# Kernel tuning notes

Measured on AMD Instinct MI355X. Metric: run time of the kernel, lower is better.

Reference implementation:

```python
import jax, jax.numpy as jnp
import numpy as np

N_NODES = 40000
N_EDGES = 640000
D_FEAT = 128
HIDDEN = 128
N_GRAPHS = 512


def setup_inputs() -> dict:
    key = jax.random.key(0)
    ks = jax.random.split(key, 6)
    x = jax.random.normal(ks[0], (N_NODES, D_FEAT), dtype=jnp.float32)
    edge_index = jax.random.randint(ks[1], (2, N_EDGES), 0, N_NODES, dtype=jnp.int32)
    batch = jnp.sort(jax.random.randint(ks[2], (N_NODES,), 0, N_GRAPHS, dtype=jnp.int32))
    s1 = 1.0 / np.sqrt(D_FEAT)
    s2 = 1.0 / np.sqrt(HIDDEN)
    W1 = jax.random.normal(ks[3], (D_FEAT, HIDDEN), dtype=jnp.float32) * s1
    b1 = jnp.zeros((HIDDEN,), dtype=jnp.float32)
    W2 = jax.random.normal(ks[4], (HIDDEN, HIDDEN), dtype=jnp.float32) * s2
    b2 = jnp.zeros((HIDDEN,), dtype=jnp.float32)
    Wfc = jax.random.normal(ks[5], (HIDDEN, 1), dtype=jnp.float32) * s2
    bfc = jnp.zeros((1,), dtype=jnp.float32)
    return {"x": x, "edge_index": edge_index, "batch": batch,
            "W1": W1, "b1": b1, "W2": W2, "b2": b2, "Wfc": Wfc, "bfc": bfc}


def _gcn_conv(x, edge_index, W, b):
    # PyG GCNConv: linear transform, add self-loops, symmetric deg^{-1/2} norm,
    # scatter-add messages from row (source) to col (target), then bias.
    n = x.shape[0]
    h = x @ W  # [N, H]
    row, col = edge_index[0], edge_index[1]
    ones = jnp.ones_like(col, dtype=h.dtype)
    deg = 1.0 + jax.ops.segment_sum(ones, col, num_segments=n)  # self-loop included
    dinv = jax.lax.rsqrt(deg)  # [N]
    norm = dinv[row] * dinv[col]  # [E]
    msg = h[row] * norm[:, None]  # [E, H]
    out = jax.ops.segment_sum(msg, col, num_segments=n)
    out = out + h * (dinv * dinv)[:, None]  # self-loop contribution
    return out + b


def _mean_pool(x, batch, num_graphs):
    sums = jax.ops.segment_sum(x, batch, num_segments=num_graphs)
    cnt = jax.ops.segment_sum(jnp.ones((x.shape[0],), dtype=x.dtype), batch, num_segments=num_graphs)
    return sums / jnp.maximum(cnt, 1.0)[:, None]


def reference(x, edge_index, batch, W1, b1, W2, b2, Wfc, bfc):
    h = jax.nn.relu(_gcn_conv(x, edge_index, W1, b1))
    h = jax.nn.relu(_gcn_conv(h, edge_index, W2, b2))
    g = _mean_pool(h, batch, N_GRAPHS)  # [G, H]
    return g @ Wfc + bfc  # [G, 1]
```

## Files before the change

### kernel.cpp

```cpp
#include <hip/hip_runtime.h>
#include <hip/hip_fp16.h>

#define N_NODES 40000
#define N_EDGES 640000
#define NFEAT   128
#define N_GRAPHS 512
#define SCAN_NB 157
#define NBKT    157
#define BKT_CAP 8192
#define BIN_BLK_EDGES 2048
#define NBLK_A ((N_EDGES + BIN_BLK_EDGES - 1) / BIN_BLK_EDGES)
#define EPAD_MAX (N_EDGES + 7 * N_NODES)

__global__ void init_misc_kernel(int* __restrict__ gcursor, int* __restrict__ gcnt,
                                 float* __restrict__ out, const float* __restrict__ bfc,
                                 __half* __restrict__ hsent) {
    int t = threadIdx.x;
    if (t <= NBKT) gcursor[t] = 0;
    float b = bfc[0];
    for (int i = t; i < N_GRAPHS; i += 256) { gcnt[i] = 0; out[i] = b; }
    if (t < NFEAT) hsent[t] = __float2half(0.0f);
}

__global__ __launch_bounds__(256) void bin_kernel(const int* __restrict__ ei,
                                                  int* __restrict__ gcursor,
                                                  unsigned int* __restrict__ binned) {
    __shared__ int lhist[NBKT];
    __shared__ int lbase[NBKT];
    const int t  = threadIdx.x;
    const int e0 = blockIdx.x * BIN_BLK_EDGES;

    if (t < NBKT) lhist[t] = 0;
    __syncthreads();

    int creg[BIN_BLK_EDGES / 256];
    #pragma unroll
    for (int i = 0; i < BIN_BLK_EDGES / 256; ++i) {
        int e = e0 + i * 256 + t;
        creg[i] = (e < N_EDGES) ? ei[N_EDGES + e] : -1;
        if (creg[i] >= 0) atomicAdd(&lhist[creg[i] >> 8], 1);
    }
    __syncthreads();

    if (t < NBKT) { lbase[t] = atomicAdd(&gcursor[t], lhist[t]); lhist[t] = 0; }
    __syncthreads();

    #pragma unroll
    for (int i = 0; i < BIN_BLK_EDGES / 256; ++i) {
        int c = creg[i];
        if (c >= 0) {
            int e = e0 + i * 256 + t;
            int r = ei[e];
            int bkt = c >> 8;
            int slot = atomicAdd(&lhist[bkt], 1);
            binned[(size_t)bkt * BKT_CAP + lbase[bkt] + slot] =
                (unsigned int)r | ((unsigned int)(c & 255) << 16);
        }
    }
}

template <typename IdxT>
__global__ __launch_bounds__(256) void bucket_build_kernel(const unsigned int* __restrict__ binned,
                                                           const int* __restrict__ gcursor,
                                                           int* __restrict__ gbase,
                                                           const int* __restrict__ batch,
                                                           int* __restrict__ gcnt,
                                                           float* __restrict__ dinv,
                                                           int* __restrict__ rowptr,
                                                           IdxT* __restrict__ csr) {
    __shared__ int chist[256];
    __shared__ int scn[256];
    __shared__ int ccur[256];
    __shared__ int ghist[N_GRAPHS];
    __shared__ int sbase;
    const int b = blockIdx.x, t = threadIdx.x;
    chist[t] = 0;
    ghist[t] = 0;
    ghist[t + 256] = 0;
    __syncthreads();
    const int cnt = gcursor[b];
    const unsigned int* src = binned + (size_t)b * BKT_CAP;
    const int col = b * 256 + t;
    const int valid = (col < N_NODES);
    if (valid) atomicAdd(&ghist[batch[col]], 1);
    for (int i = t; i < cnt; i += 256) atomicAdd(&chist[src[i] >> 16], 1);
    __syncthreads();
    int d = chist[t];
    if (valid) dinv[col] = rsqrtf(1.0f + (float)d);
    int pd = valid ? ((d + 7) & ~7) : 0;
    scn[t] = pd;
    __syncthreads();
    for (int off = 1; off < 256; off <<= 1) {
        int add = (t >= off) ? scn[t - off] : 0;
        __syncthreads();
        scn[t] += add;
        __syncthreads();
    }
    if (t == 255) sbase = atomicAdd(gbase, scn[255]);
    __syncthreads();
    const int start = sbase + scn[t] - pd;
    if (valid) rowptr[col] = start | ((pd >> 2) << 20);
    ccur[t] = start;
    __syncthreads();
    for (int i = t; i < cnt; i += 256) {
        unsigned int u = src[i];
        int slot = atomicAdd(&ccur[u >> 16], 1);
        csr[slot] = (IdxT)(u & 0xFFFFu);
    }
    __syncthreads();
    if (valid) {
        int cur = ccur[t];
        int endp = start + pd;
        for (int p = cur; p < endp; ++p) csr[p] = (IdxT)N_NODES;
    }
    int h0 = ghist[t], h1 = ghist[t + 256];
    if (h0) atomicAdd(&gcnt[t], h0);
    if (h1) atomicAdd(&gcnt[t + 256], h1);
}

__device__ inline float4 load_h4(const __half* p) {
    uint2 raw = *(const uint2*)p;
    __half2 h0 = *(__half2*)&raw.x;
    __half2 h1 = *(__half2*)&raw.y;
    float2 f0 = __half22float2(h0);
    float2 f1 = __half22float2(h1);
    return make_float4(f0.x, f0.y, f1.x, f1.y);
}
__device__ inline float4 load4v(const float* p)  { return *(const float4*)(p); }
__device__ inline float4 load4v(const __half* p) { return load_h4(p); }

__device__ inline void acc8(const uint4& raw, float* a) {
    float2 f;
    f = __half22float2(*(const __half2*)&raw.x); a[0] += f.x; a[1] += f.y;
    f = __half22float2(*(const __half2*)&raw.y); a[2] += f.x; a[3] += f.y;
    f = __half22float2(*(const __half2*)&raw.z); a[4] += f.x; a[5] += f.y;
    f = __half22float2(*(const __half2*)&raw.w); a[6] += f.x; a[7] += f.y;
}

__device__ inline int pick_q(ushort4 v, int q) {
    unsigned long long ul;
    __builtin_memcpy(&ul, &v, 8);
    return (int)((unsigned int)(ul >> (q << 4)) & 0xFFFFu);
}

template <typename InT>
__global__ __launch_bounds__(256, 4) void gemm64h_kernel(const InT* __restrict__ X,
                                                         const float* __restrict__ W,
                                                         const float* __restrict__ dinv,
                                                         __half* __restrict__ H) {
    __shared__ float Ws[128 * 64];
    const int colhalf = blockIdx.x & 1;
    const int tile    = blockIdx.x >> 1;

    for (int i = threadIdx.x; i < 2048; i += 256) {
        int k   = i >> 4;
        int cc4 = (i & 15) * 4;
        *(float4*)(Ws + k * 64 + cc4) = *(const float4*)(W + k * 128 + colhalf * 64 + cc4);
    }
    __syncthreads();

    const int rg = threadIdx.x >> 4;
    const int cg = threadIdx.x & 15;
    const int row0 = tile * 64 + rg * 4;
    const InT* x0 = X + (size_t)row0 * NFEAT;

    float acc[4][4] = {};
    float4 xc[4], xn[4];
    #pragma unroll
    for (int i = 0; i < 4; i++) xc[i] = load4v(x0 + (size_t)i * NFEAT);

    #pragma unroll 4
    for (int k = 0; k < 128; k += 4) {
        const int kn = (k + 4) & 127;
        #pragma unroll
        for (int i = 0; i < 4; i++) xn[i] = load4v(x0 + (size_t)i * NFEAT + kn);

        float4 wv[4];
        #pragma unroll
        for (int m = 0; m < 4; m++) wv[m] = *(const float4*)(Ws + (k + m) * 64 + cg * 4);

        #pragma unroll
        for (int i = 0; i < 4; i++) {
            const float xi[4] = {xc[i].x, xc[i].y, xc[i].z, xc[i].w};
            #pragma unroll
            for (int m = 0; m < 4; m++) {
                acc[i][0] += xi[m] * wv[m].x;
                acc[i][1] += xi[m] * wv[m].y;
                acc[i][2] += xi[m] * wv[m].z;
                acc[i][3] += xi[m] * wv[m].w;
            }
        }
        #pragma unroll
        for (int i = 0; i < 4; i++) xc[i] = xn[i];
    }

    #pragma unroll
    for (int i = 0; i < 4; i++) {
        float dr = dinv[row0 + i];
        __half2 p0 = __floats2half2_rn(acc[i][0] * dr, acc[i][1] * dr);
        __half2 p1 = __floats2half2_rn(acc[i][2] * dr, acc[i][3] * dr);
        uint2 pk;
        pk.x = *(unsigned int*)&p0;
        pk.y = *(unsigned int*)&p1;
        *(uint2*)(H + (size_t)(row0 + i) * NFEAT + colhalf * 64 + cg * 4) = pk;
    }
}

template <typename IdxT, typename IdxV, bool FUSE_POOL>
__global__ __launch_bounds__(256) void gather_w16_kernel(
        const int* __restrict__ rowptr, const IdxT* __restrict__ csr,
        const float* __restrict__ dinv, const __half* __restrict__ Ht,
        const float* __restrict__ bias, __half* __restrict__ outh,
        const float* __restrict__ Wfc, const int* __restrict__ batch,
        const int* __restrict__ gcnt, float* __restrict__ out, int n) {
    int gid  = blockIdx.x * blockDim.x + threadIdx.x;
    int node = __builtin_amdgcn_readfirstlane(gid >> 6);
    if (node >= n) return;
    int lane = threadIdx.x & 63;
    int q    = lane >> 4;
    int fo   = lane & 15;

    unsigned int u = (unsigned int)__builtin_amdgcn_readfirstlane(rowptr[node]);
    int start = (int)(u & 0xFFFFFu);
    int pd    = (int)(u >> 20) << 2;
    int end   = start + pd;

    float a[8] = {0.f, 0.f, 0.f, 0.f, 0.f, 0.f, 0.f, 0.f};

    if (q == 0) {
        uint4 raw = *(const uint4*)(Ht + (size_t)node * NFEAT + fo * 8);
        acc8(raw, a);
    }

    if (start < end) {
        IdxV n0 = *(const IdxV*)(csr + start);
        IdxV n1 = *(const IdxV*)(csr + start + 4);
        for (int j = start; j < end; j += 8) {
            IdxV c0 = n0, c1 = n1;
            int jn = j + 8;
            if (jn < end) {
                n0 = *(const IdxV*)(csr + jn);
                n1 = *(const IdxV*)(csr + jn + 4);
            }
            int ra = pick_q(c0, q);
            int rb = pick_q(c1, q);
            uint4 raw0 = *(const uint4*)(Ht + (size_t)ra * NFEAT + fo * 8);
            uint4 raw1 = *(const uint4*)(Ht + (size_t)rb * NFEAT + fo * 8);
            acc8(raw0, a);
            acc8(raw1, a);
        }
    }

    #pragma unroll
    for (int i = 0; i < 8; i++) {
        a[i] += __shfl_xor(a[i], 16, 64);
        a[i] += __shfl_xor(a[i], 32, 64);
    }

    float di = dinv[node];
    const float4 bb0 = *(const float4*)(bias + fo * 8);
    const float4 bb1 = *(const float4*)(bias + fo * 8 + 4);
    float o0 = fmaxf(a[0] * di + bb0.x, 0.0f);
    float o1 = fmaxf(a[1] * di + bb0.y, 0.0f);
    float o2 = fmaxf(a[2] * di + bb0.z, 0.0f);
    float o3 = fmaxf(a[3] * di + bb0.w, 0.0f);
    float o4 = fmaxf(a[4] * di + bb1.x, 0.0f);
    float o5 = fmaxf(a[5] * di + bb1.y, 0.0f);
    float o6 = fmaxf(a[6] * di + bb1.z, 0.0f);
    float o7 = fmaxf(a[7] * di + bb1.w, 0.0f);

    if (!FUSE_POOL) {
        if (q == 0) {
            __half2 p0 = __floats2half2_rn(o0, o1);
            __half2 p1 = __floats2half2_rn(o2, o3);
            __half2 p2 = __floats2half2_rn(o4, o5);
            __half2 p3 = __floats2half2_rn(o6, o7);
            uint4 pk;
            pk.x = *(unsigned int*)&p0;
            pk.y = *(unsigned int*)&p1;
            pk.z = *(unsigned int*)&p2;
            pk.w = *(unsigned int*)&p3;
            *(uint4*)(outh + (size_t)node * NFEAT + fo * 8) = pk;
        }
    } else {
        const float4 wf0 = *(const float4*)(Wfc + fo * 8);
        const float4 wf1 = *(const float4*)(Wfc + fo * 8 + 4);
        float dsum = o0 * wf0.x + o1 * wf0.y + o2 * wf0.z + o3 * wf0.w
                   + o4 * wf1.x + o5 * wf1.y + o6 * wf1.z + o7 * wf1.w;
        dsum += __shfl_xor(dsum, 1, 64);
        dsum += __shfl_xor(dsum, 2, 64);
        dsum += __shfl_xor(dsum, 4, 64);
        dsum += __shfl_xor(dsum, 8, 64);
        if (lane == 0) {
            int g = batch[node];
            int c = gcnt[g];
            float cf = (float)(c > 0 ? c : 1);
            atomicAdd(&out[g], dsum / cf);
        }
    }
}

__global__ void edge_deg_int_kernel(const int* __restrict__ ei, int* __restrict__ degcnt, int E) {
    int e = blockIdx.x * blockDim.x + threadIdx.x;
    if (e < E) atomicAdd(&degcnt[ei[E + e]], 1);
}

__global__ void dinv_from_int_kernel(const int* __restrict__ degcnt, float* __restrict__ dinv, int n) {
    int i = blockIdx.x * blockDim.x + threadIdx.x;
    if (i < n) dinv[i] = rsqrtf(1.0f + (float)degcnt[i]);
}

__global__ __launch_bounds__(256, 4) void gemm64f_kernel(const float* __restrict__ X,
                                                         const float* __restrict__ W,
                                                         const float* __restrict__ dinv,
                                                         float* __restrict__ H) {
    __shared__ float Ws[128 * 64];
    const int colhalf = blockIdx.x & 1;
    const int tile    = blockIdx.x >> 1;
    for (int i = threadIdx.x; i < 2048; i += 256) {
        int k   = i >> 4;
        int cc4 = (i & 15) * 4;
        *(float4*)(Ws + k * 64 + cc4) = *(const float4*)(W + k * 128 + colhalf * 64 + cc4);
    }
    __syncthreads();
    const int rg = threadIdx.x >> 4;
    const int cg = threadIdx.x & 15;
    const int row0 = tile * 64 + rg * 4;
    const float* x0 = X + (size_t)row0 * NFEAT;
    float acc[4][4] = {};
    #pragma unroll 4
    for (int k = 0; k < 128; k += 4) {
        float4 xv[4];
        float4 wv[4];
        #pragma unroll
        for (int i = 0; i < 4; i++) xv[i] = *(const float4*)(x0 + (size_t)i * NFEAT + k);
        #pragma unroll
        for (int m = 0; m < 4; m++) wv[m] = *(const float4*)(Ws + (k + m) * 64 + cg * 4);
        #pragma unroll
        for (int i = 0; i < 4; i++) {
            const float xi[4] = {xv[i].x, xv[i].y, xv[i].z, xv[i].w};
            #pragma unroll
            for (int m = 0; m < 4; m++) {
                acc[i][0] += xi[m] * wv[m].x;
                acc[i][1] += xi[m] * wv[m].y;
                acc[i][2] += xi[m] * wv[m].z;
                acc[i][3] += xi[m] * wv[m].w;
            }
        }
    }
    #pragma unroll
    for (int i = 0; i < 4; i++) {
        float dr = dinv[row0 + i];
        float4 o = {acc[i][0] * dr, acc[i][1] * dr, acc[i][2] * dr, acc[i][3] * dr};
        *(float4*)(H + (size_t)(row0 + i) * NFEAT + cg * 4 + colhalf * 64) = o;
    }
}

__global__ __launch_bounds__(256) void edge_scatter_kernel(const int* __restrict__ ei,
                                                           const float* __restrict__ dinv,
                                                           const float* __restrict__ H,
                                                           float* __restrict__ agg,
                                                           int E) {
    long long gid = (long long)blockIdx.x * blockDim.x + threadIdx.x;
    int e = (int)(gid >> 5);
    if (e >= E) return;
    int c4 = ((int)gid & 31) * 4;
    int r = ei[e];
    int c = ei[E + e];
    float norm = dinv[c];
    const float4 hv = *(const float4*)(H + (size_t)r * NFEAT + c4);
    float* dst = agg + (size_t)c * NFEAT + c4;
    atomicAdd(dst + 0, hv.x * norm);
    atomicAdd(dst + 1, hv.y * norm);
    atomicAdd(dst + 2, hv.z * norm);
    atomicAdd(dst + 3, hv.w * norm);
}

__global__ void post_kernel(float* __restrict__ agg, const float* __restrict__ H,
                            const float* __restrict__ dinv, const float* __restrict__ b,
                            int n) {
    int gid = blockIdx.x * blockDim.x + threadIdx.x;
    if (gid >= n * 32) return;
    int node = gid >> 5;
    int c4 = (gid & 31) * 4;
    float s = dinv[node];
    float4 a  = *(float4*)(agg + (size_t)gid * 4);
    float4 hv = *(const float4*)(H + (size_t)gid * 4);
    float4 bb = *(const float4*)(b + c4);
    float4 o;
    o.x = fmaxf(a.x + hv.x * s + bb.x, 0.0f);
    o.y = fmaxf(a.y + hv.y * s + bb.y, 0.0f);
    o.z = fmaxf(a.z + hv.z * s + bb.z, 0.0f);
    o.w = fmaxf(a.w + hv.w * s + bb.w, 0.0f);
    *(float4*)(agg + (size_t)gid * 4) = o;
}

__global__ __launch_bounds__(128) void pool_fc_kernel(const float* __restrict__ H,
                                                      const int* __restrict__ batch,
                                                      const float* __restrict__ Wfc,
                                                      const float* __restrict__ bfc,
                                                      float* __restrict__ out, int n) {
    int g = blockIdx.x;
    int tid = threadIdx.x;
    int lo = 0, hi = n;
    while (lo < hi) { int mid = (lo + hi) >> 1; if (batch[mid] < g) lo = mid + 1; else hi = mid; }
    int start = lo;
    hi = n;
    while (lo < hi) { int mid = (lo + hi) >> 1; if (batch[mid] < g + 1) lo = mid + 1; else hi = mid; }
    int end = lo;
    float acc = 0.0f;
    for (int nd = start; nd < end; ++nd) acc += H[(size_t)nd * NFEAT + tid];
    float cnt = (float)((end - start) > 0 ? (end - start) : 1);
    float v = (acc / cnt) * Wfc[tid];
    __shared__ float red[128];
    red[tid] = v;
    __syncthreads();
    #pragma unroll
    for (int s = 64; s > 0; s >>= 1) {
        if (tid < s) red[tid] += red[tid + s];
        __syncthreads();
    }
    if (tid == 0) out[g] = red[0] + bfc[0];
}

static void run_csr_path(const float* x, const int* ei, const int* batch,
                         const float* W1, const float* b1, const float* W2,
                         const float* b2, const float* Wfc, const float* bfc,
                         float* out, void* d_ws, hipStream_t stream) {
    typedef unsigned short IdxT;
    typedef ushort4 IdxV;
    char* ws = (char*)d_ws;
    const size_t hbytes = (size_t)(N_NODES + 1) * NFEAT * sizeof(__half);
    const size_t obytes = (size_t)N_NODES * NFEAT * sizeof(__half);
    __half* hbuf  = (__half*)ws;
    __half* obuf  = (__half*)(ws + hbytes);
    IdxT*   csr   = (IdxT*)(ws + hbytes + obytes);
    char*   p     = ws + hbytes + obytes + ((size_t)EPAD_MAX * sizeof(IdxT) + 15) / 16 * 16;
    int*    rowptr = (int*)p;                p += ((size_t)(N_NODES + 1) * 4 + 15) / 16 * 16;
    float*  dinv   = (float*)p;              p += ((size_t)N_NODES * 4 + 15) / 16 * 16;
    int*    gcnt   = (int*)p;

    unsigned int* binned = (unsigned int*)obuf;
    int* gcursor = (int*)(binned + (size_t)NBKT * BKT_CAP);

    init_misc_kernel<<<1, 256, 0, stream>>>(gcursor, gcnt, out, bfc,
                                            hbuf + (size_t)N_NODES * NFEAT);
    bin_kernel<<<NBLK_A, 256, 0, stream>>>(ei, gcursor, binned);
    bucket_build_kernel<IdxT><<<NBKT, 256, 0, stream>>>(binned, gcursor, gcursor + NBKT,
                                                        batch, gcnt, dinv, rowptr, csr);

    gemm64h_kernel<float><<<(N_NODES / 64) * 2, 256, 0, stream>>>(x, W1, dinv, hbuf);
    gather_w16_kernel<IdxT, IdxV, false><<<(N_NODES * 64) / 256, 256, 0, stream>>>(
        rowptr, csr, dinv, hbuf, b1, obuf, nullptr, nullptr, nullptr, nullptr, N_NODES);

    gemm64h_kernel<__half><<<(N_NODES / 64) * 2, 256, 0, stream>>>(obuf, W2, dinv, hbuf);
    gather_w16_kernel<IdxT, IdxV, true><<<(N_NODES * 64) / 256, 256, 0, stream>>>(
        rowptr, csr, dinv, hbuf, b2, nullptr, Wfc, batch, gcnt, out, N_NODES);
}

extern "C" void kernel_launch(void* const* d_in, const int* in_sizes, int n_in,
                              void* d_out, int out_size, void* d_ws, size_t ws_size,
                              hipStream_t stream) {
    const float* x     = (const float*)d_in[0];
    const int*   ei    = (const int*)  d_in[1];
    const int*   batch = (const int*)  d_in[2];
    const float* W1    = (const float*)d_in[3];
    const float* b1    = (const float*)d_in[4];
    const float* W2    = (const float*)d_in[5];
    const float* b2    = (const float*)d_in[6];
    const float* Wfc   = (const float*)d_in[7];
    const float* bfc   = (const float*)d_in[8];
    float* out = (float*)d_out;

    const size_t hbytes = (size_t)(N_NODES + 1) * NFEAT * sizeof(__half);
    const size_t obytes = (size_t)N_NODES * NFEAT * sizeof(__half);
    const size_t tail   = ((size_t)(N_NODES + 1) * 4 + 15) / 16 * 16
                        + ((size_t)N_NODES * 4 + 15) / 16 * 16
                        + (size_t)N_GRAPHS * 4;
    const size_t need = hbytes + obytes + ((size_t)EPAD_MAX * 2 + 15) / 16 * 16 + tail;

    if (ws_size >= need) {
        run_csr_path(x, ei, batch, W1, b1, W2, b2, Wfc, bfc, out, d_ws, stream);
    } else {
        float* ws   = (float*)d_ws;
        int*   degc = (int*)ws;
        float* dinv = ws + N_NODES;
        float* hbuf = ws + 2 * N_NODES;
        float* agg  = hbuf + (size_t)N_NODES * NFEAT;
        const size_t fb2 = (size_t)N_NODES * NFEAT * sizeof(float);

        hipMemsetAsync(degc, 0, (size_t)N_NODES * sizeof(int), stream);
        edge_deg_int_kernel<<<N_EDGES / 256, 256, 0, stream>>>(ei, degc, N_EDGES);
        dinv_from_int_kernel<<<SCAN_NB, 256, 0, stream>>>(degc, dinv, N_NODES);

        hipMemsetAsync(agg, 0, fb2, stream);
        gemm64f_kernel<<<(N_NODES / 64) * 2, 256, 0, stream>>>(x, W1, dinv, hbuf);
        edge_scatter_kernel<<<(N_EDGES * 32) / 256, 256, 0, stream>>>(ei, dinv, hbuf, agg, N_EDGES);
        post_kernel<<<(N_NODES * 32) / 256, 256, 0, stream>>>(agg, hbuf, dinv, b1, N_NODES);

        gemm64f_kernel<<<(N_NODES / 64) * 2, 256, 0, stream>>>(agg, W2, dinv, hbuf);
        hipMemsetAsync(agg, 0, fb2, stream);
        edge_scatter_kernel<<<(N_EDGES * 32) / 256, 256, 0, stream>>>(ei, dinv, hbuf, agg, N_EDGES);
        post_kernel<<<(N_NODES * 32) / 256, 256, 0, stream>>>(agg, hbuf, dinv, b2, N_NODES);

        pool_fc_kernel<<<N_GRAPHS, 128, 0, stream>>>(agg, batch, Wfc, bfc, out, N_NODES);
    }
}
```

Measured before the change: 276.5 us.

## Split gather kernels into four feature slabs across grid y dimension

The per-node neighbour gather now runs over four 32-feature slabs, one per blockIdx.y, with each wave handling 8 neighbours at once (8 lanes per neighbour, 4 halfs each) instead of 4 neighbours with 8 halfs per lane. This quadruples the wave count and shortens the per-node loop, aiming to raise memory-level parallelism and reduce load imbalance on high-degree nodes. In exchange, the CSR index and rowptr reads are repeated four times, each gather load shrinks to 8 bytes, and the fused pool issues four times as many atomics to the output.

Result: slower. 406.2 us (+46.9%).

```diff
diff --git a/kernel.cpp b/kernel.cpp
--- a/kernel.cpp
+++ b/kernel.cpp
@@ -11,6 +11,7 @@
 #define BIN_BLK_EDGES 2048
 #define NBLK_A ((N_EDGES + BIN_BLK_EDGES - 1) / BIN_BLK_EDGES)
 #define EPAD_MAX (N_EDGES + 7 * N_NODES)
+#define NSLAB 4
 
 __global__ void init_misc_kernel(int* __restrict__ gcursor, int* __restrict__ gcnt,
                                  float* __restrict__ out, const float* __restrict__ bfc,
@@ -129,18 +130,17 @@
 __device__ inline float4 load4v(const float* p)  { return *(const float4*)(p); }
 __device__ inline float4 load4v(const __half* p) { return load_h4(p); }
 
-__device__ inline void acc8(const uint4& raw, float* a) {
-    float2 f;
-    f = __half22float2(*(const __half2*)&raw.x); a[0] += f.x; a[1] += f.y;
-    f = __half22float2(*(const __half2*)&raw.y); a[2] += f.x; a[3] += f.y;
-    f = __half22float2(*(const __half2*)&raw.z); a[4] += f.x; a[5] += f.y;
-    f = __half22float2(*(const __half2*)&raw.w); a[6] += f.x; a[7] += f.y;
-}
-
-__device__ inline int pick_q(ushort4 v, int q) {
-    unsigned long long ul;
-    __builtin_memcpy(&ul, &v, 8);
-    return (int)((unsigned int)(ul >> (q << 4)) & 0xFFFFu);
+__device__ inline void acc4(uint2 raw, float& a0, float& a1, float& a2, float& a3) {
+    float2 f0 = __half22float2(*(__half2*)&raw.x);
+    float2 f1 = __half22float2(*(__half2*)&raw.y);
+    a0 += f0.x; a1 += f0.y; a2 += f1.x; a3 += f1.y;
+}
+
+__device__ inline int pick8(const uint4& v, int use_hi, int shift) {
+    unsigned long long lo = ((unsigned long long)v.y << 32) | (unsigned long long)v.x;
+    unsigned long long hi = ((unsigned long long)v.w << 32) | (unsigned long long)v.z;
+    unsigned long long sel = use_hi ? hi : lo;
+    return (int)((unsigned int)(sel >> shift) & 0xFFFFu);
 }
 
 template <typename InT>
@@ -206,91 +206,78 @@
     }
 }
 
-template <typename IdxT, typename IdxV, bool FUSE_POOL>
-__global__ __launch_bounds__(256) void gather_w16_kernel(
+template <typename IdxT, bool FUSE_POOL>
+__global__ __launch_bounds__(256) void gather_slab_kernel(
         const int* __restrict__ rowptr, const IdxT* __restrict__ csr,
         const float* __restrict__ dinv, const __half* __restrict__ Ht,
         const float* __restrict__ bias, __half* __restrict__ outh,
         const float* __restrict__ Wfc, const int* __restrict__ batch,
         const int* __restrict__ gcnt, float* __restrict__ out, int n) {
+    const int slab = blockIdx.y;
     int gid  = blockIdx.x * blockDim.x + threadIdx.x;
-    int node = __builtin_amdgcn_readfirstlane(gid >> 6);
+    int node = gid >> 6;
     if (node >= n) return;
     int lane = threadIdx.x & 63;
-    int q    = lane >> 4;
-    int fo   = lane & 15;
-
-    unsigned int u = (unsigned int)__builtin_amdgcn_readfirstlane(rowptr[node]);
+    int oct  = lane >> 3;
+    int fi   = lane & 7;
+    const int use_hi = oct >> 2;
+    const int shift  = (oct & 3) << 4;
+    const int fbase  = slab * 32 + fi * 4;
+    const __half* __restrict__ Hs = Ht + fbase;
+
+    unsigned int u = (unsigned int)rowptr[node];
     int start = (int)(u & 0xFFFFFu);
     int pd    = (int)(u >> 20) << 2;
     int end   = start + pd;
 
-    float a[8] = {0.f, 0.f, 0.f, 0.f, 0.f, 0.f, 0.f, 0.f};
-
-    if (q == 0) {
-        uint4 raw = *(const uint4*)(Ht + (size_t)node * NFEAT + fo * 8);
-        acc8(raw, a);
+    float a0 = 0.f, a1 = 0.f, a2 = 0.f, a3 = 0.f;
+
+    if (oct == 0) {
+        uint2 raw = *(const uint2*)(Hs + (size_t)node * NFEAT);
+        acc4(raw, a0, a1, a2, a3);
     }
 
     if (start < end) {
-        IdxV n0 = *(const IdxV*)(csr + start);
-        IdxV n1 = *(const IdxV*)(csr + start + 4);
+        uint4 iv = *(const uint4*)(csr + start);
         for (int j = start; j < end; j += 8) {
-            IdxV c0 = n0, c1 = n1;
+            uint4 cv = iv;
             int jn = j + 8;
-            if (jn < end) {
-                n0 = *(const IdxV*)(csr + jn);
-                n1 = *(const IdxV*)(csr + jn + 4);
-            }
-            int ra = pick_q(c0, q);
-            int rb = pick_q(c1, q);
-            uint4 raw0 = *(const uint4*)(Ht + (size_t)ra * NFEAT + fo * 8);
-            uint4 raw1 = *(const uint4*)(Ht + (size_t)rb * NFEAT + fo * 8);
-            acc8(raw0, a);
-            acc8(raw1, a);
-        }
-    }
-
-    #pragma unroll
-    for (int i = 0; i < 8; i++) {
-        a[i] += __shfl_xor(a[i], 16, 64);
-        a[i] += __shfl_xor(a[i], 32, 64);
-    }
+            if (jn < end) iv = *(const uint4*)(csr + jn);
+            int r = pick8(cv, use_hi, shift);
+            uint2 raw = *(const uint2*)(Hs + (size_t)r * NFEAT);
+            acc4(raw, a0, a1, a2, a3);
+        }
+    }
+
+    a0 += __shfl_xor(a0, 8, 64);  a1 += __shfl_xor(a1, 8, 64);
+    a2 += __shfl_xor(a2, 8, 64);  a3 += __shfl_xor(a3, 8, 64);
+    a0 += __shfl_xor(a0, 16, 64); a1 += __shfl_xor(a1, 16, 64);
+    a2 += __shfl_xor(a2, 16, 64); a3 += __shfl_xor(a3, 16, 64);
+    a0 += __shfl_xor(a0, 32, 64); a1 += __shfl_xor(a1, 32, 64);
+    a2 += __shfl_xor(a2, 32, 64); a3 += __shfl_xor(a3, 32, 64);
 
     float di = dinv[node];
-    const float4 bb0 = *(const float4*)(bias + fo * 8);
-    const float4 bb1 = *(const float4*)(bias + fo * 8 + 4);
-    float o0 = fmaxf(a[0] * di + bb0.x, 0.0f);
-    float o1 = fmaxf(a[1] * di + bb0.y, 0.0f);
-    float o2 = fmaxf(a[2] * di + bb0.z, 0.0f);
-    float o3 = fmaxf(a[3] * di + bb0.w, 0.0f);
-    float o4 = fmaxf(a[4] * di + bb1.x, 0.0f);
-    float o5 = fmaxf(a[5] * di + bb1.y, 0.0f);
-    float o6 = fmaxf(a[6] * di + bb1.z, 0.0f);
-    float o7 = fmaxf(a[7] * di + bb1.w, 0.0f);
+    const float4 bb = *(const float4*)(bias + fbase);
+    float o0 = fmaxf(a0 * di + bb.x, 0.0f);
+    float o1 = fmaxf(a1 * di + bb.y, 0.0f);
+    float o2 = fmaxf(a2 * di + bb.z, 0.0f);
+    float o3 = fmaxf(a3 * di + bb.w, 0.0f);
 
     if (!FUSE_POOL) {
-        if (q == 0) {
+        if (oct == 0) {
             __half2 p0 = __floats2half2_rn(o0, o1);
             __half2 p1 = __floats2half2_rn(o2, o3);
-            __half2 p2 = __floats2half2_rn(o4, o5);
-            __half2 p3 = __floats2half2_rn(o6, o7);
-            uint4 pk;
+            uint2 pk;
             pk.x = *(unsigned int*)&p0;
             pk.y = *(unsigned int*)&p1;
-            pk.z = *(unsigned int*)&p2;
-            pk.w = *(unsigned int*)&p3;
-            *(uint4*)(outh + (size_t)node * NFEAT + fo * 8) = pk;
+            *(uint2*)(outh + (size_t)node * NFEAT + fbase) = pk;
         }
     } else {
-        const float4 wf0 = *(const float4*)(Wfc + fo * 8);
-        const float4 wf1 = *(const float4*)(Wfc + fo * 8 + 4);
-        float dsum = o0 * wf0.x + o1 * wf0.y + o2 * wf0.z + o3 * wf0.w
-                   + o4 * wf1.x + o5 * wf1.y + o6 * wf1.z + o7 * wf1.w;
+        const float4 wf = *(const float4*)(Wfc + fbase);
+        float dsum = o0 * wf.x + o1 * wf.y + o2 * wf.z + o3 * wf.w;
         dsum += __shfl_xor(dsum, 1, 64);
         dsum += __shfl_xor(dsum, 2, 64);
         dsum += __shfl_xor(dsum, 4, 64);
-        dsum += __shfl_xor(dsum, 8, 64);
         if (lane == 0) {
             int g = batch[node];
             int c = gcnt[g];
@@ -428,7 +415,6 @@
                          const float* b2, const float* Wfc, const float* bfc,
                          float* out, void* d_ws, hipStream_t stream) {
     typedef unsigned short IdxT;
-    typedef ushort4 IdxV;
     char* ws = (char*)d_ws;
     const size_t hbytes = (size_t)(N_NODES + 1) * NFEAT * sizeof(__half);
     const size_t obytes = (size_t)N_NODES * NFEAT * sizeof(__half);
@@ -449,12 +435,14 @@
     bucket_build_kernel<IdxT><<<NBKT, 256, 0, stream>>>(binned, gcursor, gcursor + NBKT,
                                                         batch, gcnt, dinv, rowptr, csr);
 
+    const dim3 ggrid((N_NODES * 64) / 256, NSLAB);
+
     gemm64h_kernel<float><<<(N_NODES / 64) * 2, 256, 0, stream>>>(x, W1, dinv, hbuf);
-    gather_w16_kernel<IdxT, IdxV, false><<<(N_NODES * 64) / 256, 256, 0, stream>>>(
+    gather_slab_kernel<IdxT, false><<<ggrid, 256, 0, stream>>>(
         rowptr, csr, dinv, hbuf, b1, obuf, nullptr, nullptr, nullptr, nullptr, N_NODES);
 
     gemm64h_kernel<__half><<<(N_NODES / 64) * 2, 256, 0, stream>>>(obuf, W2, dinv, hbuf);
-    gather_w16_kernel<IdxT, IdxV, true><<<(N_NODES * 64) / 256, 256, 0, stream>>>(
+    gather_slab_kernel<IdxT, true><<<ggrid, 256, 0, stream>>>(
         rowptr, csr, dinv, hbuf, b2, nullptr, Wfc, batch, gcnt, out, N_NODES);
 }
 
```

## Fuse bucket build with first GEMM and fold init into binning

Applied to the files above, without the earlier changes.

Drops the separate init kernel: a memset plus block 0 of the bin kernel now do that zeroing. The bin kernel also counts node degrees with global atomics, so the first GEMM can compute dinv itself. That lets the bucket-build blocks and the layer-1 GEMM blocks run in one launch with a shared-memory union, cutting launches and overlapping CSR construction with the matmul. It costs 640k extra global atomics, and it removes readfirstlane hints in the gather kernel, which may cost scalarization.

Result: slower. 288.5 us (+4.3%).

```diff
diff --git a/kernel.cpp b/kernel.cpp
--- a/kernel.cpp
+++ b/kernel.cpp
@@ -11,25 +11,28 @@
 #define BIN_BLK_EDGES 2048
 #define NBLK_A ((N_EDGES + BIN_BLK_EDGES - 1) / BIN_BLK_EDGES)
 #define EPAD_MAX (N_EDGES + 7 * N_NODES)
-
-__global__ void init_misc_kernel(int* __restrict__ gcursor, int* __restrict__ gcnt,
-                                 float* __restrict__ out, const float* __restrict__ bfc,
-                                 __half* __restrict__ hsent) {
-    int t = threadIdx.x;
-    if (t <= NBKT) gcursor[t] = 0;
-    float b = bfc[0];
-    for (int i = t; i < N_GRAPHS; i += 256) { gcnt[i] = 0; out[i] = b; }
-    if (t < NFEAT) hsent[t] = __float2half(0.0f);
-}
+#define GEMM_BLKS ((N_NODES / 64) * 2)
 
 __global__ __launch_bounds__(256) void bin_kernel(const int* __restrict__ ei,
                                                   int* __restrict__ gcursor,
-                                                  unsigned int* __restrict__ binned) {
+                                                  unsigned int* __restrict__ binned,
+                                                  int* __restrict__ degcnt,
+                                                  int* __restrict__ gcnt,
+                                                  float* __restrict__ out,
+                                                  const float* __restrict__ bfc,
+                                                  __half* __restrict__ hsent) {
     __shared__ int lhist[NBKT];
     __shared__ int lbase[NBKT];
     const int t  = threadIdx.x;
     const int e0 = blockIdx.x * BIN_BLK_EDGES;
 
+    if (blockIdx.x == 0) {
+        float b = bfc[0];
+        gcnt[t] = 0; gcnt[t + 256] = 0;
+        out[t]  = b; out[t + 256]  = b;
+        if (t < NFEAT) hsent[t] = __float2half(0.0f);
+    }
+
     if (t < NBKT) lhist[t] = 0;
     __syncthreads();
 
@@ -38,7 +41,10 @@
     for (int i = 0; i < BIN_BLK_EDGES / 256; ++i) {
         int e = e0 + i * 256 + t;
         creg[i] = (e < N_EDGES) ? ei[N_EDGES + e] : -1;
-        if (creg[i] >= 0) atomicAdd(&lhist[creg[i] >> 8], 1);
+        if (creg[i] >= 0) {
+            atomicAdd(&lhist[creg[i] >> 8], 1);
+            atomicAdd(&degcnt[creg[i]], 1);
+        }
     }
     __syncthreads();
 
@@ -59,65 +65,6 @@
     }
 }
 
-template <typename IdxT>
-__global__ __launch_bounds__(256) void bucket_build_kernel(const unsigned int* __restrict__ binned,
-                                                           const int* __restrict__ gcursor,
-                                                           int* __restrict__ gbase,
-                                                           const int* __restrict__ batch,
-                                                           int* __restrict__ gcnt,
-                                                           float* __restrict__ dinv,
-                                                           int* __restrict__ rowptr,
-                                                           IdxT* __restrict__ csr) {
-    __shared__ int chist[256];
-    __shared__ int scn[256];
-    __shared__ int ccur[256];
-    __shared__ int ghist[N_GRAPHS];
-    __shared__ int sbase;
-    const int b = blockIdx.x, t = threadIdx.x;
-    chist[t] = 0;
-    ghist[t] = 0;
-    ghist[t + 256] = 0;
-    __syncthreads();
-    const int cnt = gcursor[b];
-    const unsigned int* src = binned + (size_t)b * BKT_CAP;
-    const int col = b * 256 + t;
-    const int valid = (col < N_NODES);
-    if (valid) atomicAdd(&ghist[batch[col]], 1);
-    for (int i = t; i < cnt; i += 256) atomicAdd(&chist[src[i] >> 16], 1);
-    __syncthreads();
-    int d = chist[t];
-    if (valid) dinv[col] = rsqrtf(1.0f + (float)d);
-    int pd = valid ? ((d + 7) & ~7) : 0;
-    scn[t] = pd;
-    __syncthreads();
-    for (int off = 1; off < 256; off <<= 1) {
-        int add = (t >= off) ? scn[t - off] : 0;
-        __syncthreads();
-        scn[t] += add;
-        __syncthreads();
-    }
-    if (t == 255) sbase = atomicAdd(gbase, scn[255]);
-    __syncthreads();
-    const int start = sbase + scn[t] - pd;
-    if (valid) rowptr[col] = start | ((pd >> 2) << 20);
-    ccur[t] = start;
-    __syncthreads();
-    for (int i = t; i < cnt; i += 256) {
-        unsigned int u = src[i];
-        int slot = atomicAdd(&ccur[u >> 16], 1);
-        csr[slot] = (IdxT)(u & 0xFFFFu);
-    }
-    __syncthreads();
-    if (valid) {
-        int cur = ccur[t];
-        int endp = start + pd;
-        for (int p = cur; p < endp; ++p) csr[p] = (IdxT)N_NODES;
-    }
-    int h0 = ghist[t], h1 = ghist[t + 256];
-    if (h0) atomicAdd(&gcnt[t], h0);
-    if (h1) atomicAdd(&gcnt[t + 256], h1);
-}
-
 __device__ inline float4 load_h4(const __half* p) {
     uint2 raw = *(const uint2*)p;
     __half2 h0 = *(__half2*)&raw.x;
@@ -141,6 +88,125 @@
     unsigned long long ul;
     __builtin_memcpy(&ul, &v, 8);
     return (int)((unsigned int)(ul >> (q << 4)) & 0xFFFFu);
+}
+
+template <typename IdxT>
+__global__ __launch_bounds__(256, 4) void fused_bb_gemm_kernel(
+        const unsigned int* __restrict__ binned, const int* __restrict__ gcursor,
+        int* __restrict__ gbase, const int* __restrict__ batch,
+        int* __restrict__ gcnt, float* __restrict__ dinv,
+        int* __restrict__ rowptr, IdxT* __restrict__ csr,
+        const float* __restrict__ X, const float* __restrict__ W,
+        const int* __restrict__ degcnt, __half* __restrict__ H) {
+    __shared__ union U {
+        float Ws[128 * 64];
+        struct { int chist[256]; int scn[256]; int ccur[256];
+                 int ghist[N_GRAPHS]; int sbase; } bb;
+    } lds;
+    const int t = threadIdx.x;
+
+    if (blockIdx.x < NBKT) {
+        const int b = blockIdx.x;
+        lds.bb.chist[t] = 0;
+        lds.bb.ghist[t] = 0;
+        lds.bb.ghist[t + 256] = 0;
+        __syncthreads();
+        const int cnt = gcursor[b];
+        const unsigned int* src = binned + (size_t)b * BKT_CAP;
+        const int col = b * 256 + t;
+        const int valid = (col < N_NODES);
+        if (valid) atomicAdd(&lds.bb.ghist[batch[col]], 1);
+        for (int i = t; i < cnt; i += 256) atomicAdd(&lds.bb.chist[src[i] >> 16], 1);
+        __syncthreads();
+        int d = lds.bb.chist[t];
+        if (valid) dinv[col] = rsqrtf(1.0f + (float)d);
+        int pd = valid ? ((d + 7) & ~7) : 0;
+        lds.bb.scn[t] = pd;
+        __syncthreads();
+        for (int off = 1; off < 256; off <<= 1) {
+            int add = (t >= off) ? lds.bb.scn[t - off] : 0;
+            __syncthreads();
+            lds.bb.scn[t] += add;
+            __syncthreads();
+        }
+        if (t == 255) lds.bb.sbase = atomicAdd(gbase, lds.bb.scn[255]);
+        __syncthreads();
+        const int start = lds.bb.sbase + lds.bb.scn[t] - pd;
+        if (valid) rowptr[col] = start | ((pd >> 2) << 20);
+        lds.bb.ccur[t] = start;
+        __syncthreads();
+        for (int i = t; i < cnt; i += 256) {
+            unsigned int u = src[i];
+            int slot = atomicAdd(&lds.bb.ccur[u >> 16], 1);
+            csr[slot] = (IdxT)(u & 0xFFFFu);
+        }
+        __syncthreads();
+        if (valid) {
+            int cur = lds.bb.ccur[t];
+            int endp = start + pd;
+            for (int p = cur; p < endp; ++p) csr[p] = (IdxT)N_NODES;
+        }
+        int h0 = lds.bb.ghist[t], h1 = lds.bb.ghist[t + 256];
+        if (h0) atomicAdd(&gcnt[t], h0);
+        if (h1) atomicAdd(&gcnt[t + 256], h1);
+    } else {
+        const int gb      = blockIdx.x - NBKT;
+        const int colhalf = gb & 1;
+        const int tile    = gb >> 1;
+
+        for (int i = t; i < 2048; i += 256) {
+            int k   = i >> 4;
+            int cc4 = (i & 15) * 4;
+            *(float4*)(lds.Ws + k * 64 + cc4) = *(const float4*)(W + k * 128 + colhalf * 64 + cc4);
+        }
+        __syncthreads();
+
+        const int rg = t >> 4;
+        const int cg = t & 15;
+        const int row0 = tile * 64 + rg * 4;
+        const float* x0 = X + (size_t)row0 * NFEAT;
+
+        float acc[4][4] = {};
+        float4 xc[4], xn[4];
+        #pragma unroll
+        for (int i = 0; i < 4; i++) xc[i] = load4v(x0 + (size_t)i * NFEAT);
+
+        #pragma unroll 4
+        for (int k = 0; k < 128; k += 4) {
+            const int kn = (k + 4) & 127;
+            #pragma unroll
+            for (int i = 0; i < 4; i++) xn[i] = load4v(x0 + (size_t)i * NFEAT + kn);
+
+            float4 wv[4];
+            #pragma unroll
+            for (int m = 0; m < 4; m++) wv[m] = *(const float4*)(lds.Ws + (k + m) * 64 + cg * 4);
+
+            #pragma unroll
+            for (int i = 0; i < 4; i++) {
+                const float xi[4] = {xc[i].x, xc[i].y, xc[i].z, xc[i].w};
+                #pragma unroll
+                for (int m = 0; m < 4; m++) {
+                    acc[i][0] += xi[m] * wv[m].x;
+                    acc[i][1] += xi[m] * wv[m].y;
+                    acc[i][2] += xi[m] * wv[m].z;
+                    acc[i][3] += xi[m] * wv[m].w;
+                }
+            }
+            #pragma unroll
+            for (int i = 0; i < 4; i++) xc[i] = xn[i];
+        }
+
+        #pragma unroll
+        for (int i = 0; i < 4; i++) {
+            float dr = rsqrtf(1.0f + (float)degcnt[row0 + i]);
+            __half2 p0 = __floats2half2_rn(acc[i][0] * dr, acc[i][1] * dr);
+            __half2 p1 = __floats2half2_rn(acc[i][2] * dr, acc[i][3] * dr);
+            uint2 pk;
+            pk.x = *(unsigned int*)&p0;
+            pk.y = *(unsigned int*)&p1;
+            *(uint2*)(H + (size_t)(row0 + i) * NFEAT + colhalf * 64 + cg * 4) = pk;
+        }
+    }
 }
 
 template <typename InT>
@@ -214,13 +280,13 @@
         const float* __restrict__ Wfc, const int* __restrict__ batch,
         const int* __restrict__ gcnt, float* __restrict__ out, int n) {
     int gid  = blockIdx.x * blockDim.x + threadIdx.x;
-    int node = __builtin_amdgcn_readfirstlane(gid >> 6);
+    int node = gid >> 6;
     if (node >= n) return;
     int lane = threadIdx.x & 63;
     int q    = lane >> 4;
     int fo   = lane & 15;
 
-    unsigned int u = (unsigned int)__builtin_amdgcn_readfirstlane(rowptr[node]);
+    unsigned int u = (unsigned int)rowptr[node];
     int start = (int)(u & 0xFFFFFu);
     int pd    = (int)(u >> 20) << 2;
     int end   = start + pd;
@@ -442,18 +508,22 @@
 
     unsigned int* binned = (unsigned int*)obuf;
     int* gcursor = (int*)(binned + (size_t)NBKT * BKT_CAP);
-
-    init_misc_kernel<<<1, 256, 0, stream>>>(gcursor, gcnt, out, bfc,
-                                            hbuf + (size_t)N_NODES * NFEAT);
-    bin_kernel<<<NBLK_A, 256, 0, stream>>>(ei, gcursor, binned);
-    bucket_build_kernel<IdxT><<<NBKT, 256, 0, stream>>>(binned, gcursor, gcursor + NBKT,
-                                                        batch, gcnt, dinv, rowptr, csr);
-
-    gemm64h_kernel<float><<<(N_NODES / 64) * 2, 256, 0, stream>>>(x, W1, dinv, hbuf);
+    int* degcnt  = gcursor + 160;
+
+    hipMemsetAsync(gcursor, 0, (size_t)(160 + N_NODES) * sizeof(int), stream);
+
+    bin_kernel<<<NBLK_A, 256, 0, stream>>>(ei, gcursor, binned, degcnt, gcnt,
+                                           out, bfc, hbuf + (size_t)N_NODES * NFEAT);
+
+    fused_bb_gemm_kernel<IdxT><<<NBKT + GEMM_BLKS, 256, 0, stream>>>(
+        binned, gcursor, gcursor + NBKT, batch, gcnt, dinv, rowptr, csr,
+        x, W1, degcnt, hbuf);
+
     gather_w16_kernel<IdxT, IdxV, false><<<(N_NODES * 64) / 256, 256, 0, stream>>>(
         rowptr, csr, dinv, hbuf, b1, obuf, nullptr, nullptr, nullptr, nullptr, N_NODES);
 
-    gemm64h_kernel<__half><<<(N_NODES / 64) * 2, 256, 0, stream>>>(obuf, W2, dinv, hbuf);
+    gemm64h_kernel<__half><<<GEMM_BLKS, 256, 0, stream>>>(obuf, W2, dinv, hbuf);
+
     gather_w16_kernel<IdxT, IdxV, true><<<(N_NODES * 64) / 256, 256, 0, stream>>>(
         rowptr, csr, dinv, hbuf, b2, nullptr, Wfc, batch, gcnt, out, N_NODES);
 }
```
